# Kernel optimization log

Hardware: AMD Instinct MI355X
Metric: run time of the kernel (lower is better)

## Reference

```python
import jax, jax.numpy as jnp
import numpy as np
import math

IN_C = 1024
OUT_C = 1024
HEADS = 16
GROUPS = 4

def grouped_linear(src, weight, bias):
    # src: [..., in_c]; weight: [g, in_c//g, out_c//g]; bias: [out_c]
    g, icg, ocg = weight.shape
    lead = src.shape[:-1]
    s = src.reshape(*lead, g, icg)
    out = jnp.einsum('...gi,gio->...go', s, weight)
    out = out.reshape(*lead, g * ocg)
    return out + bias

def restricted_softmax(src, margin=0.0):
    src_max = jnp.maximum(jnp.max(src, axis=-1, keepdims=True), 0.0)
    out = jnp.exp(src - src_max)
    return out / (jnp.sum(out, axis=-1, keepdims=True) + jnp.exp(margin - src_max))

def setup_inputs() -> dict:
    key = jax.random.key(0)
    ks = jax.random.split(key, 9)
    B, S = 2, 2048
    icg, ocg = IN_C // GROUPS, OUT_C // GROUPS
    scale = 1.0 / math.sqrt(icg)
    return {
        'query': jax.random.normal(ks[0], (B, S, IN_C), jnp.float32),
        'key': jax.random.normal(ks[1], (B, S, IN_C), jnp.float32),
        'value': jax.random.normal(ks[2], (B, S, IN_C), jnp.float32),
        'wq': jax.random.uniform(ks[3], (GROUPS, icg, ocg), jnp.float32, -scale, scale),
        'wk': jax.random.uniform(ks[4], (GROUPS, icg, ocg), jnp.float32, -scale, scale),
        'wv': jax.random.uniform(ks[5], (GROUPS, icg, ocg), jnp.float32, -scale, scale),
        'bq': jax.random.uniform(ks[6], (OUT_C,), jnp.float32, -scale, scale),
        'bk': jax.random.uniform(ks[7], (OUT_C,), jnp.float32, -scale, scale),
        'bv': jax.random.uniform(ks[8], (OUT_C,), jnp.float32, -scale, scale),
    }

def reference(query, key, value, wq, wk, wv, bq, bk, bv):
    q = grouped_linear(query, wq, bq)   # [B,S,OUT_C]
    k = grouped_linear(key, wk, bk)
    v = grouped_linear(value, wv, bv)
    B, Sq, _ = q.shape
    Sk = k.shape[-2]
    d = OUT_C // HEADS
    q = q.reshape(B, Sq, HEADS, d).transpose(0, 2, 1, 3)  # [B,H,Sq,d]
    k = k.reshape(B, Sk, HEADS, d).transpose(0, 2, 1, 3)
    v = v.reshape(B, Sk, HEADS, d).transpose(0, 2, 1, 3)
    score = jnp.einsum('bhqd,bhkd->bhqk', q, k) / math.sqrt(d)
    attn = restricted_softmax(score)
    out = jnp.einsum('bhqk,bhkd->bhqd', attn, v)
    out = out.transpose(0, 2, 1, 3).reshape(B, Sq, OUT_C)
    return out
```

## Files before the change

### kernel.cpp

```cpp
#include <hip/hip_runtime.h>
#include <hip/hip_bf16.h>

#define BB 2
#define SS 2048
#define CC 1024
#define HH 16
#define DDIM 64
#define NROWS (BB*SS)

#define QSC 0.18033688011112042f

typedef __attribute__((ext_vector_type(8))) short bf16x8;
typedef __attribute__((ext_vector_type(4))) float f32x4;

__device__ __forceinline__ f32x4 mfma16(bf16x8 a, bf16x8 b, f32x4 c) {
    return __builtin_amdgcn_mfma_f32_16x16x32_bf16(a, b, c, 0, 0, 0);
}

__global__ __launch_bounds__(256) void prep_wt(
    const float* __restrict__ wq, const float* __restrict__ wk,
    const float* __restrict__ wv, __hip_bfloat16* __restrict__ wt)
{
    const float* w = blockIdx.z == 0 ? wq : blockIdx.z == 1 ? wk : wv;
    const int g  = blockIdx.y;
    const int kt = blockIdx.x >> 2;
    const int nt = blockIdx.x & 3;
    __shared__ __hip_bfloat16 Ls[64][72];
    const int t = threadIdx.x;
    #pragma unroll
    for (int j = 0; j < 4; ++j) {
        int f4 = t + j*256;
        int row = f4 >> 4, n0 = (f4 & 15) * 4;
        float4 f = *(const float4*)&w[(size_t)g*65536 + (size_t)(kt*64+row)*256
                                      + nt*64 + n0];
        Ls[n0+0][row] = __float2bfloat16(f.x);
        Ls[n0+1][row] = __float2bfloat16(f.y);
        Ls[n0+2][row] = __float2bfloat16(f.z);
        Ls[n0+3][row] = __float2bfloat16(f.w);
    }
    __syncthreads();
    #pragma unroll
    for (int j = 0; j < 2; ++j) {
        int u = t + j*256;
        int nr = u >> 3, k8 = (u & 7) * 8;
        *(uint4*)&wt[((size_t)(blockIdx.z*4 + g)*256 + nt*64 + nr)*256
                     + kt*64 + k8] = *(const uint4*)&Ls[nr][k8];
    }
}

__global__ __launch_bounds__(256, 4) void proj_mfma(
    const float* __restrict__ qin, const float* __restrict__ kin,
    const float* __restrict__ vin,
    const __hip_bfloat16* __restrict__ wt,
    const float* __restrict__ bq, const float* __restrict__ bk,
    const float* __restrict__ bv,
    __hip_bfloat16* __restrict__ qs, __hip_bfloat16* __restrict__ ks_,
    __hip_bfloat16* __restrict__ vs)
{
    const int z = blockIdx.z;
    const float* src; const float* bias;
    if (z == 0)      { src = qin; bias = bq; }
    else if (z == 1) { src = kin; bias = bk; }
    else             { src = vin; bias = bv; }

    const int h    = blockIdx.y;
    const int g    = h >> 2;
    const int col0 = (h & 3) * 64;
    const int row0 = blockIdx.x * 128;
    const int b    = row0 >> 11;
    const int s0   = row0 & 2047;

    __shared__ char smemA[128*72*2];
    __shared__ __hip_bfloat16 Ws[64][72];
    auto As = (__hip_bfloat16 (*)[72])smemA;

    const int t    = threadIdx.x;
    const int wid  = t >> 6;
    const int lane = t & 63;
    const int l16  = lane & 15;
    const int quad = lane >> 4;

    f32x4 acc[2][4];
    #pragma unroll
    for (int mt = 0; mt < 2; ++mt)
        #pragma unroll
        for (int nt = 0; nt < 4; ++nt) acc[mt][nt] = (f32x4){0.f,0.f,0.f,0.f};

    const __hip_bfloat16* wtz = wt + (size_t)(z*4 + g)*65536 + (size_t)col0*256;

    for (int kt = 0; kt < 4; ++kt) {
        __syncthreads();
        #pragma unroll
        for (int j = 0; j < 8; ++j) {
            int idx = t + j*256;
            int row = idx >> 4, c4 = (idx & 15) * 4;
            float4 f = *(const float4*)&src[(size_t)(row0 + row)*CC + g*256
                                            + kt*64 + c4];
            union { __hip_bfloat16 hh[4]; uint2 u; } pk;
            pk.hh[0] = __float2bfloat16(f.x); pk.hh[1] = __float2bfloat16(f.y);
            pk.hh[2] = __float2bfloat16(f.z); pk.hh[3] = __float2bfloat16(f.w);
            *(uint2*)&As[row][c4] = pk.u;
        }
        #pragma unroll
        for (int j = 0; j < 2; ++j) {
            int idx = t + j*256;
            int n = idx >> 3, k8 = (idx & 7) * 8;
            *(uint4*)&Ws[n][k8] =
                *(const uint4*)&wtz[(size_t)n*256 + kt*64 + k8];
        }
        __syncthreads();
        #pragma unroll
        for (int kss = 0; kss < 2; ++kss) {
            bf16x8 af[2], wf[4];
            #pragma unroll
            for (int mt = 0; mt < 2; ++mt)
                af[mt] = *(const bf16x8*)&As[wid*32 + mt*16 + l16][kss*32 + quad*8];
            #pragma unroll
            for (int nt = 0; nt < 4; ++nt)
                wf[nt] = *(const bf16x8*)&Ws[nt*16 + l16][kss*32 + quad*8];
            #pragma unroll
            for (int mt = 0; mt < 2; ++mt)
                #pragma unroll
                for (int nt = 0; nt < 4; ++nt)
                    acc[mt][nt] = mfma16(af[mt], wf[nt], acc[mt][nt]);
        }
    }

    float bval[4];
    #pragma unroll
    for (int nt = 0; nt < 4; ++nt) bval[nt] = bias[g*256 + col0 + nt*16 + l16];

    __syncthreads();

    if (z < 2) {
        const float scale = (z == 0) ? QSC : 1.0f;
        auto Ot = (__hip_bfloat16 (*)[72])smemA;
        #pragma unroll
        for (int mt = 0; mt < 2; ++mt)
            #pragma unroll
            for (int nt = 0; nt < 4; ++nt)
                #pragma unroll
                for (int r = 0; r < 4; ++r)
                    Ot[wid*32 + mt*16 + quad*4 + r][nt*16 + l16] =
                        __float2bfloat16((acc[mt][nt][r] + bval[nt]) * scale);
        __syncthreads();
        __hip_bfloat16* dst = ((z == 0) ? qs : ks_) + ((size_t)(b*HH + h) << 17);
        #pragma unroll
        for (int j = 0; j < 4; ++j) {
            int f = wid + j*4;
            int t16 = f >> 1, kcs = f & 1;
            uint4 v = *(const uint4*)&Ot[t16*16 + l16][kcs*32 + quad*8];
            *(uint4*)&dst[((size_t)((((s0 >> 4) + t16)*2 + kcs)) << 9) + lane*8] = v;
        }
    } else {
        auto Vl = (__hip_bfloat16 (*)[136])smemA;
        #pragma unroll
        for (int mt = 0; mt < 2; ++mt)
            #pragma unroll
            for (int nt = 0; nt < 4; ++nt) {
                union { __hip_bfloat16 hh[4]; uint2 u; } pk;
                #pragma unroll
                for (int r = 0; r < 4; ++r)
                    pk.hh[r] = __float2bfloat16(acc[mt][nt][r] + bval[nt]);
                *(uint2*)&Vl[nt*16 + l16][wid*32 + mt*16 + quad*4] = pk.u;
            }
        __syncthreads();
        __hip_bfloat16* dst = vs + ((size_t)(b*HH + h) << 17);
        const int kc0 = s0 >> 5;
        #pragma unroll
        for (int j = 0; j < 4; ++j) {
            int f = wid + j*4;
            int dt = f >> 2, kcl = f & 3;
            uint4 v = *(const uint4*)&Vl[dt*16 + l16][kcl*32 + quad*8];
            *(uint4*)&dst[((size_t)(dt*64 + kc0 + kcl) << 9) + lane*8] = v;
        }
    }
}

__global__ __launch_bounds__(256, 2) void attn_mfma(
    const __hip_bfloat16* __restrict__ qs, const __hip_bfloat16* __restrict__ ks_,
    const __hip_bfloat16* __restrict__ vs, float* __restrict__ out)
{
    const int qt = blockIdx.x;
    const int h  = blockIdx.y;
    const int b  = blockIdx.z;

    __shared__ __hip_bfloat16 Ps[4][32][72];

    const int t    = threadIdx.x;
    const int wid  = t >> 6;
    const int lane = t & 63;
    const int l16  = lane & 15;
    const int quad = lane >> 4;

    const __hip_bfloat16* qb = qs + ((size_t)(b*HH + h) << 17);
    const __hip_bfloat16* kb = ks_ + ((size_t)(b*HH + h) << 17);
    const __hip_bfloat16* vb = vs + ((size_t)(b*HH + h) << 17);

    bf16x8 qf[2][2];
    #pragma unroll
    for (int mt = 0; mt < 2; ++mt)
        #pragma unroll
        for (int kss = 0; kss < 2; ++kss)
            qf[mt][kss] = *(const bf16x8*)(qb +
                ((size_t)((qt*8 + wid*2 + mt)*2 + kss) << 9) + lane*8);

    f32x4 O[2][4];
    float Lacc[2] = {0.f, 0.f};
    #pragma unroll
    for (int mt = 0; mt < 2; ++mt)
        #pragma unroll
        for (int dt = 0; dt < 4; ++dt) O[mt][dt] = (f32x4){0.f,0.f,0.f,0.f};

    bf16x8 kf[4][2];
    #pragma unroll
    for (int nt = 0; nt < 4; ++nt)
        #pragma unroll
        for (int kss = 0; kss < 2; ++kss)
            kf[nt][kss] = *(const bf16x8*)(kb +
                ((size_t)(nt*2 + kss) << 9) + lane*8);

    for (int kt = 0; kt < SS/64; ++kt) {
        bf16x8 vf[4][2];
        #pragma unroll
        for (int dt = 0; dt < 4; ++dt)
            #pragma unroll
            for (int kss = 0; kss < 2; ++kss)
                vf[dt][kss] = *(const bf16x8*)(vb +
                    ((size_t)(dt*64 + kt*2 + kss) << 9) + lane*8);

        f32x4 st[4][2];
        #pragma unroll
        for (int nt = 0; nt < 4; ++nt)
            #pragma unroll
            for (int mt = 0; mt < 2; ++mt) {
                f32x4 z = (f32x4){0.f,0.f,0.f,0.f};
                z = mfma16(kf[nt][0], qf[mt][0], z);
                st[nt][mt] = mfma16(kf[nt][1], qf[mt][1], z);
            }

        if (kt + 1 < SS/64) {
            #pragma unroll
            for (int nt = 0; nt < 4; ++nt)
                #pragma unroll
                for (int kss = 0; kss < 2; ++kss)
                    kf[nt][kss] = *(const bf16x8*)(kb +
                        ((size_t)((kt+1)*8 + nt*2 + kss) << 9) + lane*8);
        }

        #pragma unroll
        for (int nt = 0; nt < 4; ++nt)
            #pragma unroll
            for (int mt = 0; mt < 2; ++mt) {
                union { __hip_bfloat16 hh[4]; uint2 u; } pk;
                #pragma unroll
                for (int r = 0; r < 4; ++r) {
                    float p = __builtin_amdgcn_exp2f(st[nt][mt][r]);
                    Lacc[mt] += p;
                    pk.hh[r] = __float2bfloat16(p);
                }
                *(uint2*)&Ps[wid][mt*16 + l16][nt*16 + quad*4] = pk.u;
            }

        bf16x8 pf[2][2];
        #pragma unroll
        for (int mt = 0; mt < 2; ++mt)
            #pragma unroll
            for (int kss = 0; kss < 2; ++kss)
                pf[mt][kss] = *(const bf16x8*)&Ps[wid][mt*16 + l16][kss*32 + quad*8];

        #pragma unroll
        for (int dt = 0; dt < 4; ++dt)
            #pragma unroll
            for (int mt = 0; mt < 2; ++mt) {
                O[mt][dt] = mfma16(vf[dt][0], pf[mt][0], O[mt][dt]);
                O[mt][dt] = mfma16(vf[dt][1], pf[mt][1], O[mt][dt]);
            }
    }

    const int qrow0 = qt*128 + wid*32;
    #pragma unroll
    for (int mt = 0; mt < 2; ++mt) {
        float Lr = Lacc[mt];
        Lr += __shfl_xor(Lr, 16);
        Lr += __shfl_xor(Lr, 32);
        const float inv = 1.0f / (1.0f + Lr);
        const size_t row = (size_t)b*SS + qrow0 + mt*16 + l16;
        #pragma unroll
        for (int dt = 0; dt < 4; ++dt) {
            float4 o4;
            o4.x = O[mt][dt][0] * inv;
            o4.y = O[mt][dt][1] * inv;
            o4.z = O[mt][dt][2] * inv;
            o4.w = O[mt][dt][3] * inv;
            *(float4*)&out[row*CC + h*DDIM + dt*16 + quad*4] = o4;
        }
    }
}

extern "C" void kernel_launch(void* const* d_in, const int* in_sizes, int n_in,
                              void* d_out, int out_size, void* d_ws, size_t ws_size,
                              hipStream_t stream) {
    (void)in_sizes; (void)n_in; (void)out_size; (void)ws_size;
    const float* qin = (const float*)d_in[0];
    const float* kin = (const float*)d_in[1];
    const float* vin = (const float*)d_in[2];
    const float* wq  = (const float*)d_in[3];
    const float* wk  = (const float*)d_in[4];
    const float* wv  = (const float*)d_in[5];
    const float* bq  = (const float*)d_in[6];
    const float* bk  = (const float*)d_in[7];
    const float* bv  = (const float*)d_in[8];

    __hip_bfloat16* qs = (__hip_bfloat16*)d_ws;
    __hip_bfloat16* ks = qs + (size_t)NROWS*CC;
    __hip_bfloat16* vs = ks + (size_t)NROWS*CC;
    __hip_bfloat16* wt = vs + (size_t)NROWS*CC;
    float* out = (float*)d_out;

    prep_wt<<<dim3(16, 4, 3), 256, 0, stream>>>(wq, wk, wv, wt);
    proj_mfma<<<dim3(32, 16, 3), 256, 0, stream>>>(
        qin, kin, vin, wt, bq, bk, bv, qs, ks, vs);
    attn_mfma<<<dim3(16, 16, 2), 256, 0, stream>>>(qs, ks, vs, out);
}
```

Measured before the change: 178.7 us.

## Split attention keys across two blocks, widen projection tiles, and add combine pass

The attention kernel now splits the key sequence in half, so twice as many blocks run. Each half writes unnormalized partial outputs and row sums, and a new combine kernel merges and normalizes them. Row sums are now computed with an MFMA against a ones vector instead of scalar adds plus shuffles. The projection kernel now computes 128 output columns per block, covering two heads, which halves its grid and raises reuse of the activation tile. The cost is an extra kernel launch and a large fp32 partial buffer that must be written and read back, plus more registers per projection block.

```diff
diff --git a/kernel.cpp b/kernel.cpp
--- a/kernel.cpp
+++ b/kernel.cpp
@@ -48,7 +48,7 @@
     }
 }
 
-__global__ __launch_bounds__(256, 4) void proj_mfma(
+__global__ __launch_bounds__(256, 3) void proj_mfma(
     const float* __restrict__ qin, const float* __restrict__ kin,
     const float* __restrict__ vin,
     const __hip_bfloat16* __restrict__ wt,
@@ -63,16 +63,16 @@
     else if (z == 1) { src = kin; bias = bk; }
     else             { src = vin; bias = bv; }
 
-    const int h    = blockIdx.y;
-    const int g    = h >> 2;
-    const int col0 = (h & 3) * 64;
+    const int hp   = blockIdx.y;
+    const int g    = hp >> 1;
+    const int col0 = (hp & 1) * 128;
     const int row0 = blockIdx.x * 128;
     const int b    = row0 >> 11;
     const int s0   = row0 & 2047;
 
-    __shared__ char smemA[128*72*2];
-    __shared__ __hip_bfloat16 Ws[64][72];
-    auto As = (__hip_bfloat16 (*)[72])smemA;
+    __shared__ char smem[36864];
+    auto As = (__hip_bfloat16 (*)[72])smem;
+    auto Ws = (__hip_bfloat16 (*)[72])(smem + 18432);
 
     const int t    = threadIdx.x;
     const int wid  = t >> 6;
@@ -80,13 +80,13 @@
     const int l16  = lane & 15;
     const int quad = lane >> 4;
 
-    f32x4 acc[2][4];
+    f32x4 acc[2][8];
     #pragma unroll
     for (int mt = 0; mt < 2; ++mt)
         #pragma unroll
-        for (int nt = 0; nt < 4; ++nt) acc[mt][nt] = (f32x4){0.f,0.f,0.f,0.f};
-
-    const __hip_bfloat16* wtz = wt + (size_t)(z*4 + g)*65536 + (size_t)col0*256;
+        for (int nt = 0; nt < 8; ++nt) acc[mt][nt] = (f32x4){0.f,0.f,0.f,0.f};
+
+    const __hip_bfloat16* wtz = wt + (size_t)(z*4 + g)*65536;
 
     for (int kt = 0; kt < 4; ++kt) {
         __syncthreads();
@@ -102,62 +102,65 @@
             *(uint2*)&As[row][c4] = pk.u;
         }
         #pragma unroll
-        for (int j = 0; j < 2; ++j) {
+        for (int j = 0; j < 4; ++j) {
             int idx = t + j*256;
             int n = idx >> 3, k8 = (idx & 7) * 8;
             *(uint4*)&Ws[n][k8] =
-                *(const uint4*)&wtz[(size_t)n*256 + kt*64 + k8];
+                *(const uint4*)&wtz[(size_t)(col0 + n)*256 + kt*64 + k8];
         }
         __syncthreads();
         #pragma unroll
         for (int kss = 0; kss < 2; ++kss) {
-            bf16x8 af[2], wf[4];
+            bf16x8 af[2], wf[8];
             #pragma unroll
             for (int mt = 0; mt < 2; ++mt)
                 af[mt] = *(const bf16x8*)&As[wid*32 + mt*16 + l16][kss*32 + quad*8];
             #pragma unroll
-            for (int nt = 0; nt < 4; ++nt)
+            for (int nt = 0; nt < 8; ++nt)
                 wf[nt] = *(const bf16x8*)&Ws[nt*16 + l16][kss*32 + quad*8];
             #pragma unroll
             for (int mt = 0; mt < 2; ++mt)
                 #pragma unroll
-                for (int nt = 0; nt < 4; ++nt)
+                for (int nt = 0; nt < 8; ++nt)
                     acc[mt][nt] = mfma16(af[mt], wf[nt], acc[mt][nt]);
         }
     }
 
-    float bval[4];
-    #pragma unroll
-    for (int nt = 0; nt < 4; ++nt) bval[nt] = bias[g*256 + col0 + nt*16 + l16];
+    float bval[8];
+    #pragma unroll
+    for (int nt = 0; nt < 8; ++nt) bval[nt] = bias[g*256 + col0 + nt*16 + l16];
 
     __syncthreads();
 
     if (z < 2) {
         const float scale = (z == 0) ? QSC : 1.0f;
-        auto Ot = (__hip_bfloat16 (*)[72])smemA;
+        auto Ot = (__hip_bfloat16 (*)[136])smem;
         #pragma unroll
         for (int mt = 0; mt < 2; ++mt)
             #pragma unroll
-            for (int nt = 0; nt < 4; ++nt)
+            for (int nt = 0; nt < 8; ++nt)
                 #pragma unroll
                 for (int r = 0; r < 4; ++r)
                     Ot[wid*32 + mt*16 + quad*4 + r][nt*16 + l16] =
                         __float2bfloat16((acc[mt][nt][r] + bval[nt]) * scale);
         __syncthreads();
-        __hip_bfloat16* dst = ((z == 0) ? qs : ks_) + ((size_t)(b*HH + h) << 17);
-        #pragma unroll
-        for (int j = 0; j < 4; ++j) {
+        __hip_bfloat16* base = (z == 0) ? qs : ks_;
+        #pragma unroll
+        for (int j = 0; j < 8; ++j) {
             int f = wid + j*4;
-            int t16 = f >> 1, kcs = f & 1;
-            uint4 v = *(const uint4*)&Ot[t16*16 + l16][kcs*32 + quad*8];
-            *(uint4*)&dst[((size_t)((((s0 >> 4) + t16)*2 + kcs)) << 9) + lane*8] = v;
+            int hl = f >> 4, t16l = (f >> 1) & 7, kcs = f & 1;
+            uint4 v = *(const uint4*)&Ot[t16l*16 + l16][hl*64 + kcs*32 + quad*8];
+            int h = hp*2 + hl;
+            int t16g = (s0 >> 4) + t16l;
+            *(uint4*)&base[((size_t)(b*HH + h) << 17)
+                           + ((size_t)(t16g*2 + kcs) << 9) + lane*8] = v;
         }
     } else {
-        auto Vl = (__hip_bfloat16 (*)[136])smemA;
+        auto Vl = (__hip_bfloat16 (*)[136])smem;
         #pragma unroll
         for (int mt = 0; mt < 2; ++mt)
             #pragma unroll
-            for (int nt = 0; nt < 4; ++nt) {
+            for (int nt = 0; nt < 8; ++nt) {
                 union { __hip_bfloat16 hh[4]; uint2 u; } pk;
                 #pragma unroll
                 for (int r = 0; r < 4; ++r)
@@ -165,25 +168,28 @@
                 *(uint2*)&Vl[nt*16 + l16][wid*32 + mt*16 + quad*4] = pk.u;
             }
         __syncthreads();
-        __hip_bfloat16* dst = vs + ((size_t)(b*HH + h) << 17);
         const int kc0 = s0 >> 5;
         #pragma unroll
-        for (int j = 0; j < 4; ++j) {
+        for (int j = 0; j < 8; ++j) {
             int f = wid + j*4;
-            int dt = f >> 2, kcl = f & 3;
-            uint4 v = *(const uint4*)&Vl[dt*16 + l16][kcl*32 + quad*8];
-            *(uint4*)&dst[((size_t)(dt*64 + kc0 + kcl) << 9) + lane*8] = v;
-        }
-    }
-}
-
-__global__ __launch_bounds__(256, 2) void attn_mfma(
+            int hl = f >> 4, dt = (f >> 2) & 3, kcl = f & 3;
+            uint4 v = *(const uint4*)&Vl[hl*64 + dt*16 + l16][kcl*32 + quad*8];
+            int h = hp*2 + hl;
+            *(uint4*)&vs[((size_t)(b*HH + h) << 17)
+                         + ((size_t)(dt*64 + kc0 + kcl) << 9) + lane*8] = v;
+        }
+    }
+}
+
+__global__ __launch_bounds__(256, 3) void attn_mfma(
     const __hip_bfloat16* __restrict__ qs, const __hip_bfloat16* __restrict__ ks_,
-    const __hip_bfloat16* __restrict__ vs, float* __restrict__ out)
+    const __hip_bfloat16* __restrict__ vs, float* __restrict__ out,
+    float* __restrict__ U1, float* __restrict__ L0, float* __restrict__ L1)
 {
-    const int qt = blockIdx.x;
-    const int h  = blockIdx.y;
-    const int b  = blockIdx.z;
+    const int half = blockIdx.x >> 4;
+    const int qt   = blockIdx.x & 15;
+    const int h    = blockIdx.y;
+    const int b    = blockIdx.z;
 
     __shared__ __hip_bfloat16 Ps[4][32][72];
 
@@ -197,6 +203,9 @@
     const __hip_bfloat16* kb = ks_ + ((size_t)(b*HH + h) << 17);
     const __hip_bfloat16* vb = vs + ((size_t)(b*HH + h) << 17);
 
+    const bf16x8 onesv = (bf16x8){16256,16256,16256,16256,
+                                  16256,16256,16256,16256};
+
     bf16x8 qf[2][2];
     #pragma unroll
     for (int mt = 0; mt < 2; ++mt)
@@ -206,21 +215,27 @@
                 ((size_t)((qt*8 + wid*2 + mt)*2 + kss) << 9) + lane*8);
 
     f32x4 O[2][4];
-    float Lacc[2] = {0.f, 0.f};
-    #pragma unroll
-    for (int mt = 0; mt < 2; ++mt)
+    f32x4 Lfrag[2];
+    #pragma unroll
+    for (int mt = 0; mt < 2; ++mt) {
+        Lfrag[mt] = (f32x4){0.f,0.f,0.f,0.f};
         #pragma unroll
         for (int dt = 0; dt < 4; ++dt) O[mt][dt] = (f32x4){0.f,0.f,0.f,0.f};
-
+    }
+
+    const int kt0 = half * 16;
     bf16x8 kf[4][2];
     #pragma unroll
     for (int nt = 0; nt < 4; ++nt)
         #pragma unroll
         for (int kss = 0; kss < 2; ++kss)
             kf[nt][kss] = *(const bf16x8*)(kb +
-                ((size_t)(nt*2 + kss) << 9) + lane*8);
-
-    for (int kt = 0; kt < SS/64; ++kt) {
+                ((size_t)(kt0*8 + nt*2 + kss) << 9) + lane*8);
+
+    #pragma unroll
+    for (int i = 0; i < 16; ++i) {
+        const int kt = kt0 + i;
+
         bf16x8 vf[4][2];
         #pragma unroll
         for (int dt = 0; dt < 4; ++dt)
@@ -239,7 +254,7 @@
                 st[nt][mt] = mfma16(kf[nt][1], qf[mt][1], z);
             }
 
-        if (kt + 1 < SS/64) {
+        if (i < 15) {
             #pragma unroll
             for (int nt = 0; nt < 4; ++nt)
                 #pragma unroll
@@ -254,11 +269,9 @@
             for (int mt = 0; mt < 2; ++mt) {
                 union { __hip_bfloat16 hh[4]; uint2 u; } pk;
                 #pragma unroll
-                for (int r = 0; r < 4; ++r) {
-                    float p = __builtin_amdgcn_exp2f(st[nt][mt][r]);
-                    Lacc[mt] += p;
-                    pk.hh[r] = __float2bfloat16(p);
-                }
+                for (int r = 0; r < 4; ++r)
+                    pk.hh[r] = __float2bfloat16(
+                        __builtin_amdgcn_exp2f(st[nt][mt][r]));
                 *(uint2*)&Ps[wid][mt*16 + l16][nt*16 + quad*4] = pk.u;
             }
 
@@ -268,6 +281,12 @@
             #pragma unroll
             for (int kss = 0; kss < 2; ++kss)
                 pf[mt][kss] = *(const bf16x8*)&Ps[wid][mt*16 + l16][kss*32 + quad*8];
+
+        #pragma unroll
+        for (int mt = 0; mt < 2; ++mt) {
+            Lfrag[mt] = mfma16(onesv, pf[mt][0], Lfrag[mt]);
+            Lfrag[mt] = mfma16(onesv, pf[mt][1], Lfrag[mt]);
+        }
 
         #pragma unroll
         for (int dt = 0; dt < 4; ++dt)
@@ -278,24 +297,38 @@
             }
     }
 
+    float* dstU = (half == 0) ? out : U1;
+    float* dstL = (half == 0) ? L0 : L1;
     const int qrow0 = qt*128 + wid*32;
     #pragma unroll
     for (int mt = 0; mt < 2; ++mt) {
-        float Lr = Lacc[mt];
-        Lr += __shfl_xor(Lr, 16);
-        Lr += __shfl_xor(Lr, 32);
-        const float inv = 1.0f / (1.0f + Lr);
         const size_t row = (size_t)b*SS + qrow0 + mt*16 + l16;
+        if (quad == 0) dstL[row*HH + h] = Lfrag[mt][0];
         #pragma unroll
         for (int dt = 0; dt < 4; ++dt) {
             float4 o4;
-            o4.x = O[mt][dt][0] * inv;
-            o4.y = O[mt][dt][1] * inv;
-            o4.z = O[mt][dt][2] * inv;
-            o4.w = O[mt][dt][3] * inv;
-            *(float4*)&out[row*CC + h*DDIM + dt*16 + quad*4] = o4;
-        }
-    }
+            o4.x = O[mt][dt][0]; o4.y = O[mt][dt][1];
+            o4.z = O[mt][dt][2]; o4.w = O[mt][dt][3];
+            *(float4*)&dstU[row*CC + h*DDIM + dt*16 + quad*4] = o4;
+        }
+    }
+}
+
+__global__ __launch_bounds__(256) void combine(
+    float* __restrict__ out, const float* __restrict__ U1,
+    const float* __restrict__ L0, const float* __restrict__ L1)
+{
+    const int idx = blockIdx.x*256 + threadIdx.x;
+    const int row = idx >> 8;
+    const int c4  = (idx & 255) * 4;
+    const int h   = c4 >> 6;
+    const float inv = 1.0f / (1.0f + L0[row*HH + h] + L1[row*HH + h]);
+    float4 a = *(const float4*)&out[(size_t)idx*4];
+    float4 u = *(const float4*)&U1[(size_t)idx*4];
+    float4 o;
+    o.x = (a.x + u.x)*inv; o.y = (a.y + u.y)*inv;
+    o.z = (a.z + u.z)*inv; o.w = (a.w + u.w)*inv;
+    *(float4*)&out[(size_t)idx*4] = o;
 }
 
 extern "C" void kernel_launch(void* const* d_in, const int* in_sizes, int n_in,
@@ -312,14 +345,19 @@
     const float* bk  = (const float*)d_in[7];
     const float* bv  = (const float*)d_in[8];
 
-    __hip_bfloat16* qs = (__hip_bfloat16*)d_ws;
-    __hip_bfloat16* ks = qs + (size_t)NROWS*CC;
-    __hip_bfloat16* vs = ks + (size_t)NROWS*CC;
-    __hip_bfloat16* wt = vs + (size_t)NROWS*CC;
+    char* w0 = (char*)d_ws;
+    __hip_bfloat16* qs = (__hip_bfloat16*)(w0);
+    __hip_bfloat16* ks = (__hip_bfloat16*)(w0 + 8388608);
+    __hip_bfloat16* vs = (__hip_bfloat16*)(w0 + 16777216);
+    __hip_bfloat16* wt = (__hip_bfloat16*)(w0 + 25165824);
+    float* U1 = (float*)(w0 + 26738688);
+    float* L0 = (float*)(w0 + 43515904);
+    float* L1 = (float*)(w0 + 43778048);
     float* out = (float*)d_out;
 
     prep_wt<<<dim3(16, 4, 3), 256, 0, stream>>>(wq, wk, wv, wt);
-    proj_mfma<<<dim3(32, 16, 3), 256, 0, stream>>>(
+    proj_mfma<<<dim3(32, 8, 3), 256, 0, stream>>>(
         qin, kin, vin, wt, bq, bk, bv, qs, ks, vs);
-    attn_mfma<<<dim3(16, 16, 2), 256, 0, stream>>>(qs, ks, vs, out);
-}
+    attn_mfma<<<dim3(32, 16, 2), 256, 0, stream>>>(qs, ks, vs, out, U1, L0, L1);
+    combine<<<dim3(4096), 256, 0, stream>>>(out, U1, L0, L1);
+}
```

Measured after the change: 177.1 us. About the same (-0.9%).
